# Kernel optimization log

Measured on AMD Instinct MI355X. Metric: run time of the kernel, lower is better.

## Reference

```python
import jax, jax.numpy as jnp
import numpy as np

L = 16384
D = 1024   # input_size
A = 1024   # attention_size


def setup_inputs() -> dict:
    key = jax.random.key(0)
    k1, k2, k3, k4, k5 = jax.random.split(key, 5)
    return {
        "h_i": jax.random.normal(k1, (L, D), dtype=jnp.float32),
        "h_t": jax.random.normal(k2, (1, D), dtype=jnp.float32),
        "W_att": jax.random.normal(k3, (A, 2 * D), dtype=jnp.float32) * (1.0 / np.sqrt(2 * D)),
        "b_att": jax.random.normal(k4, (A,), dtype=jnp.float32) * 0.01,
        "u": jax.random.normal(k5, (A, 1), dtype=jnp.float32),
    }


def reference(h_i, h_t, W_att, b_att, u):
    # m_combine = tanh(Linear(cat([h_i, repeat(h_t)], dim=1)))  -> [L, A]
    ht_rep = jnp.broadcast_to(h_t, h_i.shape)                  # [L, D]
    m = jnp.tanh(jnp.concatenate([h_i, ht_rep], axis=1) @ W_att.T + b_att)
    beta = (m @ u).T                                           # [1, L]
    alpha = jax.nn.softmax(beta, axis=1)                       # [1, L]
    s = alpha @ h_i                                            # [1, D]
    return s
```

## Files before the change

kernel.cpp:

```cpp
#include <hip/hip_runtime.h>
#include <hip/hip_fp16.h>


#define L_ROWS 16384
#define D_DIM  1024
#define A_DIM  1024

typedef _Float16 f16;
typedef _Float16 f16x4 __attribute__((ext_vector_type(4)));
typedef _Float16 f16x8 __attribute__((ext_vector_type(8)));
typedef float    f32x4 __attribute__((ext_vector_type(4)));

__device__ __forceinline__ void gload_lds16(const void* g, void* l) {
  __builtin_amdgcn_global_load_lds(
      (const __attribute__((address_space(1))) void*)g,
      (__attribute__((address_space(3))) void*)l,
      16, 0, 0);
}

__device__ __forceinline__ float fast_tanh(float x) {
  float e = exp2f(x * 2.885390081777927f);
  return 1.0f - 2.0f * __builtin_amdgcn_rcpf(e + 1.0f);
}

__global__ void k_conv_h(const float* __restrict__ src, f16* __restrict__ dst) {
  const int idx = blockIdx.x * blockDim.x + threadIdx.x;
  float4 v = reinterpret_cast<const float4*>(src)[idx];
  f16x4 o; o.x = (f16)v.x; o.y = (f16)v.y; o.z = (f16)v.z; o.w = (f16)v.w;
  reinterpret_cast<f16x4*>(dst)[idx] = o;
}

__global__ void k_conv_w(const float* __restrict__ Watt, f16* __restrict__ W16) {
  const int idx = blockIdx.x * blockDim.x + threadIdx.x;
  const int a  = idx >> 8;
  const int c4 = idx & 255;
  float4 v = reinterpret_cast<const float4*>(Watt)[(size_t)a * 512 + c4];
  f16x4 o; o.x = (f16)v.x; o.y = (f16)v.y; o.z = (f16)v.z; o.w = (f16)v.w;
  reinterpret_cast<f16x4*>(W16)[a * 256 + c4] = o;
}

__global__ void k_c(const float* __restrict__ Watt, const float* __restrict__ ht,
                    const float* __restrict__ b, float* __restrict__ c) {
  const int a = blockIdx.x * 4 + (threadIdx.x >> 6);
  const int lane = threadIdx.x & 63;
  const float* row = Watt + (size_t)a * 2048 + 1024;
  float s = 0.f;
  #pragma unroll
  for (int d = lane; d < 1024; d += 64) s += row[d] * ht[d];
  #pragma unroll
  for (int off = 32; off; off >>= 1) s += __shfl_down(s, off);
  if (lane == 0) c[a] = s;
}

__global__ __launch_bounds__(256, 3)
void k_gemm(const f16* __restrict__ H, const f16* __restrict__ W,
            const float* __restrict__ u, const float* __restrict__ c,
            float* __restrict__ betap) {
  __shared__ __align__(16) f16 As[128][32];
  __shared__ __align__(16) f16 Bs[128][32];
  __shared__ float red[128];

  const int tid  = threadIdx.x;
  const int bx   = blockIdx.x;
  const int by   = blockIdx.y;
  const int brow = by * 128;
  const int bcol = bx * 128;

  const int w    = tid >> 6;
  const int lane = tid & 63;
  const int wm   = w >> 1, wn = w & 1;
  const int lg   = lane >> 4;
  const int ll   = lane & 15;

  f32x4 acc[4][4] = {};

  const int srow = tid >> 2;
  const int scol = (tid & 3) * 8;
  const f16* gA = H + (size_t)(brow + srow) * D_DIM + scol;
  const f16* gB = W + (size_t)(bcol + srow) * D_DIM + scol;
  char* lA = (char*)(&As[0][0]) + tid * 16;
  char* lB = (char*)(&Bs[0][0]) + tid * 16;

  for (int kt = 0; kt < D_DIM / 32; ++kt) {
    const int ko = kt * 32;
    gload_lds16(gA + ko,              lA);
    gload_lds16(gA + ko + 64 * D_DIM, lA + 4096);
    gload_lds16(gB + ko,              lB);
    gload_lds16(gB + ko + 64 * D_DIM, lB + 4096);
    __syncthreads();

    f16x8 af[4], bf[4];
    #pragma unroll
    for (int m = 0; m < 4; ++m)
      af[m] = *(const f16x8*)&As[wm * 64 + m * 16 + ll][lg * 8];
    #pragma unroll
    for (int n = 0; n < 4; ++n)
      bf[n] = *(const f16x8*)&Bs[wn * 64 + n * 16 + ll][lg * 8];
    #pragma unroll
    for (int m = 0; m < 4; ++m)
      #pragma unroll
      for (int n = 0; n < 4; ++n)
        acc[m][n] = __builtin_amdgcn_mfma_f32_16x16x32_f16(af[m], bf[n], acc[m][n], 0, 0, 0);
    __syncthreads();
  }

  float uv[4], cv[4];
  #pragma unroll
  for (int n = 0; n < 4; ++n) {
    const int a = bcol + wn * 64 + n * 16 + ll;
    uv[n] = u[a];
    cv[n] = c[a];
  }
  if (tid < 128) red[tid] = 0.f;
  __syncthreads();

  #pragma unroll
  for (int m = 0; m < 4; ++m) {
    float rs[4] = {0.f, 0.f, 0.f, 0.f};
    #pragma unroll
    for (int n = 0; n < 4; ++n) {
      #pragma unroll
      for (int r = 0; r < 4; ++r) {
        const float z = acc[m][n][r] + cv[n];
        rs[r] += fast_tanh(z) * uv[n];
      }
    }
    #pragma unroll
    for (int r = 0; r < 4; ++r) {
      float v = rs[r];
      v += __shfl_xor(v, 1);
      v += __shfl_xor(v, 2);
      v += __shfl_xor(v, 4);
      v += __shfl_xor(v, 8);
      if (ll == 0) atomicAdd(&red[wm * 64 + m * 16 + lg * 4 + r], v);
    }
  }
  __syncthreads();
  if (tid < 128) betap[(size_t)bx * L_ROWS + brow + tid] = red[tid];
}

__global__ __launch_bounds__(1024)
void k_softmax(const float* __restrict__ betap, float* __restrict__ alpha) {
  __shared__ float sred[32];
  const int t = threadIdx.x;
  float e[16];
  float mx = -3.0e38f;
  #pragma unroll
  for (int i = 0; i < 16; ++i) {
    const int l = t + i * 1024;
    float bsum = 0.f;
    #pragma unroll
    for (int j = 0; j < 8; ++j) bsum += betap[j * L_ROWS + l];
    e[i] = bsum;
    mx = fmaxf(mx, bsum);
  }
  #pragma unroll
  for (int off = 32; off; off >>= 1) mx = fmaxf(mx, __shfl_xor(mx, off));
  if ((t & 63) == 0) sred[t >> 6] = mx;
  __syncthreads();
  #pragma unroll
  for (int wv = 0; wv < 16; ++wv) mx = fmaxf(mx, sred[wv]);
  __syncthreads();
  float ssum = 0.f;
  #pragma unroll
  for (int i = 0; i < 16; ++i) {
    e[i] = expf(e[i] - mx);
    ssum += e[i];
  }
  #pragma unroll
  for (int off = 32; off; off >>= 1) ssum += __shfl_xor(ssum, off);
  if ((t & 63) == 0) sred[t >> 6] = ssum;
  __syncthreads();
  float tot = 0.f;
  #pragma unroll
  for (int wv = 0; wv < 16; ++wv) tot += sred[wv];
  const float rinv = 1.0f / tot;
  #pragma unroll
  for (int i = 0; i < 16; ++i) alpha[t + i * 1024] = e[i] * rinv;
}

__global__ __launch_bounds__(256)
void k_spart(const float* __restrict__ hi, const float* __restrict__ alpha,
             float* __restrict__ spart) {
  const int t  = threadIdx.x;
  const int wg = blockIdx.x;
  const int r0 = wg * 64;
  float4 accv = make_float4(0.f, 0.f, 0.f, 0.f);
  const float4* hp = reinterpret_cast<const float4*>(hi + (size_t)r0 * D_DIM) + t;
  #pragma unroll 4
  for (int r = 0; r < 64; ++r) {
    const float a = alpha[r0 + r];
    float4 h = hp[r * 256];
    accv.x += a * h.x; accv.y += a * h.y; accv.z += a * h.z; accv.w += a * h.w;
  }
  reinterpret_cast<float4*>(spart + (size_t)wg * D_DIM)[t] = accv;
}

__global__ __launch_bounds__(256)
void k_sred(const float* __restrict__ spart, float* __restrict__ out) {
  const int col = blockIdx.x * 256 + threadIdx.x;
  float s = 0.f;
  for (int p = 0; p < 256; ++p) s += spart[p * D_DIM + col];
  out[col] = s;
}

extern "C" void kernel_launch(void* const* d_in, const int* in_sizes, int n_in,
                              void* d_out, int out_size, void* d_ws, size_t ws_size,
                              hipStream_t stream) {
  (void)in_sizes; (void)n_in; (void)out_size; (void)ws_size;
  const float* h_i = (const float*)d_in[0];
  const float* h_t = (const float*)d_in[1];
  const float* W   = (const float*)d_in[2];
  const float* b   = (const float*)d_in[3];
  const float* u   = (const float*)d_in[4];
  float* out = (float*)d_out;

  char* ws = (char*)d_ws;
  f16*   h16   = (f16*)ws;
  f16*   W16   = (f16*)(ws + 33554432);
  float* cvec  = (float*)(ws + 35651584);
  float* betap = (float*)(ws + 35655680);
  float* alpha = (float*)(ws + 36179968);
  float* spart = (float*)(ws + 36245504);

  k_conv_h<<<16384, 256, 0, stream>>>(h_i, h16);
  k_conv_w<<<1024, 256, 0, stream>>>(W, W16);
  k_c<<<256, 256, 0, stream>>>(W, h_t, b, cvec);
  k_gemm<<<dim3(8, 128), 256, 0, stream>>>(h16, W16, u, cvec, betap);
  k_softmax<<<1, 1024, 0, stream>>>(betap, alpha);
  k_spart<<<256, 256, 0, stream>>>(h_i, alpha, spart);
  k_sred<<<4, 256, 0, stream>>>(spart, out);
}
```

Baseline: 219.4 us.

## Parallelize softmax across blocks, read fp16 h in weighted sum, reshape grids

Replaces the single-block softmax with a 16-block pass that writes per-block max and sum, and merges those stats inside the weighted-sum kernel. The weighted sum now reads the fp16 copy of h over 1024 blocks, and the final reduction spreads over 64 blocks. It also swaps the GEMM grid order, converts h with a strided loop, and adds the missing bias to c. The aim is to remove serial single-block tails and halve memory traffic in the weighted sum, at some precision cost from using fp16 h.

```diff
diff --git a/kernel.cpp b/kernel.cpp
--- a/kernel.cpp
+++ b/kernel.cpp
@@ -23,15 +23,22 @@
   return 1.0f - 2.0f * __builtin_amdgcn_rcpf(e + 1.0f);
 }
 
-__global__ void k_conv_h(const float* __restrict__ src, f16* __restrict__ dst) {
-  const int idx = blockIdx.x * blockDim.x + threadIdx.x;
-  float4 v = reinterpret_cast<const float4*>(src)[idx];
-  f16x4 o; o.x = (f16)v.x; o.y = (f16)v.y; o.z = (f16)v.z; o.w = (f16)v.w;
-  reinterpret_cast<f16x4*>(dst)[idx] = o;
-}
-
-__global__ void k_conv_w(const float* __restrict__ Watt, f16* __restrict__ W16) {
-  const int idx = blockIdx.x * blockDim.x + threadIdx.x;
+__global__ __launch_bounds__(256)
+void k_conv_h(const float* __restrict__ src, f16* __restrict__ dst) {
+  const float4* s4 = reinterpret_cast<const float4*>(src);
+  f16x4* d4 = reinterpret_cast<f16x4*>(dst);
+  int i = blockIdx.x * 256 + threadIdx.x;
+  #pragma unroll
+  for (int it = 0; it < 8; ++it, i += 524288) {
+    float4 v = s4[i];
+    f16x4 o; o.x = (f16)v.x; o.y = (f16)v.y; o.z = (f16)v.z; o.w = (f16)v.w;
+    d4[i] = o;
+  }
+}
+
+__global__ __launch_bounds__(256)
+void k_conv_w(const float* __restrict__ Watt, f16* __restrict__ W16) {
+  const int idx = blockIdx.x * 256 + threadIdx.x;
   const int a  = idx >> 8;
   const int c4 = idx & 255;
   float4 v = reinterpret_cast<const float4*>(Watt)[(size_t)a * 512 + c4];
@@ -39,8 +46,9 @@
   reinterpret_cast<f16x4*>(W16)[a * 256 + c4] = o;
 }
 
-__global__ void k_c(const float* __restrict__ Watt, const float* __restrict__ ht,
-                    const float* __restrict__ b, float* __restrict__ c) {
+__global__ __launch_bounds__(256)
+void k_c(const float* __restrict__ Watt, const float* __restrict__ ht,
+         const float* __restrict__ b, float* __restrict__ c) {
   const int a = blockIdx.x * 4 + (threadIdx.x >> 6);
   const int lane = threadIdx.x & 63;
   const float* row = Watt + (size_t)a * 2048 + 1024;
@@ -49,7 +57,7 @@
   for (int d = lane; d < 1024; d += 64) s += row[d] * ht[d];
   #pragma unroll
   for (int off = 32; off; off >>= 1) s += __shfl_down(s, off);
-  if (lane == 0) c[a] = s;
+  if (lane == 0) c[a] = b[a] + s;
 }
 
 __global__ __launch_bounds__(256, 3)
@@ -61,9 +69,8 @@
   __shared__ float red[128];
 
   const int tid  = threadIdx.x;
-  const int bx   = blockIdx.x;
-  const int by   = blockIdx.y;
-  const int brow = by * 128;
+  const int brow = blockIdx.x * 128;
+  const int bx   = blockIdx.y;
   const int bcol = bx * 128;
 
   const int w    = tid >> 6;
@@ -140,68 +147,82 @@
 }
 
 __global__ __launch_bounds__(1024)
-void k_softmax(const float* __restrict__ betap, float* __restrict__ alpha) {
-  __shared__ float sred[32];
+void k_smax(const float* __restrict__ betap, float* __restrict__ beta,
+            float* __restrict__ stats) {
+  __shared__ float sred[16];
   const int t = threadIdx.x;
-  float e[16];
-  float mx = -3.0e38f;
-  #pragma unroll
-  for (int i = 0; i < 16; ++i) {
-    const int l = t + i * 1024;
-    float bsum = 0.f;
-    #pragma unroll
-    for (int j = 0; j < 8; ++j) bsum += betap[j * L_ROWS + l];
-    e[i] = bsum;
-    mx = fmaxf(mx, bsum);
-  }
+  const int r = blockIdx.x * 1024 + t;
+  float bsum = 0.f;
+  #pragma unroll
+  for (int j = 0; j < 8; ++j) bsum += betap[j * L_ROWS + r];
+  beta[r] = bsum;
+  float mx = bsum;
   #pragma unroll
   for (int off = 32; off; off >>= 1) mx = fmaxf(mx, __shfl_xor(mx, off));
   if ((t & 63) == 0) sred[t >> 6] = mx;
   __syncthreads();
-  #pragma unroll
-  for (int wv = 0; wv < 16; ++wv) mx = fmaxf(mx, sred[wv]);
-  __syncthreads();
-  float ssum = 0.f;
-  #pragma unroll
-  for (int i = 0; i < 16; ++i) {
-    e[i] = expf(e[i] - mx);
-    ssum += e[i];
-  }
-  #pragma unroll
-  for (int off = 32; off; off >>= 1) ssum += __shfl_xor(ssum, off);
-  if ((t & 63) == 0) sred[t >> 6] = ssum;
-  __syncthreads();
-  float tot = 0.f;
-  #pragma unroll
-  for (int wv = 0; wv < 16; ++wv) tot += sred[wv];
-  const float rinv = 1.0f / tot;
-  #pragma unroll
-  for (int i = 0; i < 16; ++i) alpha[t + i * 1024] = e[i] * rinv;
-}
-
-__global__ __launch_bounds__(256)
-void k_spart(const float* __restrict__ hi, const float* __restrict__ alpha,
-             float* __restrict__ spart) {
+  float bm = sred[0];
+  #pragma unroll
+  for (int wv = 1; wv < 16; ++wv) bm = fmaxf(bm, sred[wv]);
+  __syncthreads();
+  float e = expf(bsum - bm);
+  float s = e;
+  #pragma unroll
+  for (int off = 32; off; off >>= 1) s += __shfl_xor(s, off);
+  if ((t & 63) == 0) sred[t >> 6] = s;
+  __syncthreads();
+  if (t == 0) {
+    float tot = 0.f;
+    #pragma unroll
+    for (int wv = 0; wv < 16; ++wv) tot += sred[wv];
+    stats[blockIdx.x] = bm;
+    stats[16 + blockIdx.x] = tot;
+  }
+}
+
+__global__ __launch_bounds__(256)
+void k_spart(const f16* __restrict__ h16, const float* __restrict__ beta,
+             const float* __restrict__ stats, float* __restrict__ spart) {
+  float gmax = stats[0];
+  #pragma unroll
+  for (int j = 1; j < 16; ++j) gmax = fmaxf(gmax, stats[j]);
+  float gsum = 0.f;
+  #pragma unroll
+  for (int j = 0; j < 16; ++j) gsum += stats[16 + j] * expf(stats[j] - gmax);
+  const float rg = 1.0f / gsum;
+
   const int t  = threadIdx.x;
-  const int wg = blockIdx.x;
-  const int r0 = wg * 64;
-  float4 accv = make_float4(0.f, 0.f, 0.f, 0.f);
-  const float4* hp = reinterpret_cast<const float4*>(hi + (size_t)r0 * D_DIM) + t;
-  #pragma unroll 4
-  for (int r = 0; r < 64; ++r) {
-    const float a = alpha[r0 + r];
-    float4 h = hp[r * 256];
-    accv.x += a * h.x; accv.y += a * h.y; accv.z += a * h.z; accv.w += a * h.w;
-  }
-  reinterpret_cast<float4*>(spart + (size_t)wg * D_DIM)[t] = accv;
+  const int r0 = blockIdx.x * 16;
+  float4 acc = make_float4(0.f, 0.f, 0.f, 0.f);
+  const f16x4* hp = reinterpret_cast<const f16x4*>(h16 + (size_t)r0 * D_DIM) + t;
+  #pragma unroll
+  for (int r = 0; r < 16; ++r) {
+    const float a = expf(beta[r0 + r] - gmax) * rg;
+    f16x4 h = hp[r * 256];
+    acc.x += a * (float)h.x; acc.y += a * (float)h.y;
+    acc.z += a * (float)h.z; acc.w += a * (float)h.w;
+  }
+  reinterpret_cast<float4*>(spart + (size_t)blockIdx.x * D_DIM)[t] = acc;
 }
 
 __global__ __launch_bounds__(256)
 void k_sred(const float* __restrict__ spart, float* __restrict__ out) {
-  const int col = blockIdx.x * 256 + threadIdx.x;
+  __shared__ float red[256];
+  const int tid = threadIdx.x;
+  const int c = tid & 15;
+  const int g = tid >> 4;
+  const int col = blockIdx.x * 16 + c;
   float s = 0.f;
-  for (int p = 0; p < 256; ++p) s += spart[p * D_DIM + col];
-  out[col] = s;
+  #pragma unroll 8
+  for (int p = g; p < 1024; p += 16) s += spart[(size_t)p * D_DIM + col];
+  red[tid] = s;
+  __syncthreads();
+  if (tid < 16) {
+    float tot = 0.f;
+    #pragma unroll
+    for (int g2 = 0; g2 < 16; ++g2) tot += red[g2 * 16 + tid];
+    out[blockIdx.x * 16 + tid] = tot;
+  }
 }
 
 extern "C" void kernel_launch(void* const* d_in, const int* in_sizes, int n_in,
@@ -220,14 +241,15 @@
   f16*   W16   = (f16*)(ws + 33554432);
   float* cvec  = (float*)(ws + 35651584);
   float* betap = (float*)(ws + 35655680);
-  float* alpha = (float*)(ws + 36179968);
-  float* spart = (float*)(ws + 36245504);
-
-  k_conv_h<<<16384, 256, 0, stream>>>(h_i, h16);
+  float* beta  = (float*)(ws + 36179968);
+  float* stats = (float*)(ws + 36245504);
+  float* spart = (float*)(ws + 36245632);
+
+  k_conv_h<<<2048, 256, 0, stream>>>(h_i, h16);
   k_conv_w<<<1024, 256, 0, stream>>>(W, W16);
   k_c<<<256, 256, 0, stream>>>(W, h_t, b, cvec);
-  k_gemm<<<dim3(8, 128), 256, 0, stream>>>(h16, W16, u, cvec, betap);
-  k_softmax<<<1, 1024, 0, stream>>>(betap, alpha);
-  k_spart<<<256, 256, 0, stream>>>(h_i, alpha, spart);
-  k_sred<<<4, 256, 0, stream>>>(spart, out);
-}
+  k_gemm<<<dim3(128, 8), 256, 0, stream>>>(h16, W16, u, cvec, betap);
+  k_smax<<<16, 1024, 0, stream>>>(betap, beta, stats);
+  k_spart<<<1024, 256, 0, stream>>>(h16, beta, stats, spart);
+  k_sred<<<64, 256, 0, stream>>>(spart, out);
+}
```

After: 184.5 us. -15.9%, faster.
